# Kernel optimization log

Hardware: AMD Instinct MI355X
Metric: run time of the kernel (lower is better)

## Reference

```python
import jax, jax.numpy as jnp
import numpy as np

d_model = 512


def setup_inputs() -> dict:
    key = jax.random.key(0)
    k1, k2, k3, k4 = jax.random.split(key, 4)
    B, T, d_k = 8, 2048, 64
    scale = 1.0 / np.sqrt(d_model)
    x = jax.random.normal(k1, (B, T, d_model), dtype=jnp.float32)
    Wk = jax.random.normal(k2, (d_model, d_k), dtype=jnp.float32) * scale
    Wq = jax.random.normal(k3, (d_model, d_k), dtype=jnp.float32) * scale
    Wv = jax.random.normal(k4, (d_model, d_k), dtype=jnp.float32) * scale
    return {"x": x, "Wk": Wk, "Wq": Wq, "Wv": Wv}


def reference(x, Wk, Wq, Wv):
    # x: [B,T,C]; W*: [C,d_k]  (torch Linear weight is [d_k,C]; we store transposed)
    k = jnp.einsum('btc,cd->btd', x, Wk)
    q = jnp.einsum('btc,cd->btd', x, Wq)
    v = jnp.einsum('btc,cd->btd', x, Wv)
    d_k = k.shape[-1]
    scores = jnp.einsum('bqd,bkd->bqk', q, k) / jnp.sqrt(jnp.float32(d_k))
    attn = jax.nn.softmax(scores, axis=-1)  # [B,T,T]
    return jnp.einsum('bqk,bkd->bqd', attn, v)
```

## Files before the change

### kernel.cpp

```cpp
#include <hip/hip_runtime.h>
#include <hip/hip_bf16.h>
#include <stdint.h>


typedef short bf16x8 __attribute__((ext_vector_type(8)));
typedef float f32x4 __attribute__((ext_vector_type(4)));

#define MFMA_BF16 __builtin_amdgcn_mfma_f32_16x16x32_bf16

__device__ __forceinline__ unsigned int pk2(float a, float b) {
    __hip_bfloat162 h = __float22bfloat162_rn(float2{a, b});
    union { __hip_bfloat162 h; unsigned int u; } r; r.h = h;
    return r.u;
}

__device__ __forceinline__ uint2 pack4_bf16(float a, float b, float c, float d) {
    uint2 r; r.x = pk2(a, b); r.y = pk2(c, d); return r;
}

__device__ __forceinline__ bf16x8 cvt8(f32x4 a, f32x4 b) {
    union { bf16x8 v; unsigned int u[4]; } r;
    r.u[0] = pk2(a[0], a[1]); r.u[1] = pk2(a[2], a[3]);
    r.u[2] = pk2(b[0], b[1]); r.u[3] = pk2(b[2], b[3]);
    return r.v;
}

__device__ __forceinline__ unsigned short bf1(float a) {
    __hip_bfloat16 h = __float2bfloat16(a);
    union { __hip_bfloat16 h; unsigned short u; } r; r.h = h;
    return r.u;
}

__global__ void wt_kernel(const float* __restrict__ Wq,
                          const float* __restrict__ Wk,
                          const float* __restrict__ Wv,
                          unsigned short* __restrict__ wt2)
{
    int id = blockIdx.x * 256 + threadIdx.x;
    int c    = id & 15;
    int quad = (id >> 4) & 3;
    int ks   = (id >> 6) & 15;
    int mt   = (id >> 10) & 3;
    int w    = id >> 12;
    const float* src = (w == 0) ? Wq : ((w == 1) ? Wk : Wv);
    const int n  = mt * 16 + c;
    const int k0 = ks * 32 + quad * 8;
    unsigned short* dst = wt2 + (size_t)id * 8;
    #pragma unroll
    for (int j = 0; j < 8; j++)
        dst[j] = bf1(src[(size_t)(k0 + j) * 64 + n]);
}

__global__ __launch_bounds__(256, 1) void proj_kernel(
    const float* __restrict__ x, const unsigned short* __restrict__ wt2,
    unsigned short* __restrict__ qg, unsigned short* __restrict__ kg2,
    unsigned short* __restrict__ vg2)
{
    __shared__ unsigned short xs[32768];

    const int tid  = threadIdx.x;
    const int lane = tid & 63;
    const int wave = tid >> 6;
    const int c    = lane & 15;
    const int quad = lane >> 4;
    const int tt   = blockIdx.x;
    const int t0   = tt * 64;

    const float* xb = x + (size_t)tt * 32768;
    #pragma unroll
    for (int t = 0; t < 16; t++) {
        int i = t * 256 + tid;
        f32x4 a = *(const f32x4*)(xb + (size_t)i * 8);
        f32x4 b = *(const f32x4*)(xb + (size_t)i * 8 + 4);
        int tok = i >> 6;
        int db  = i & 63;
        *(bf16x8*)(xs + ((size_t)db * 64 + (tok ^ (db & 7))) * 8) = cvt8(a, b);
    }
    __syncthreads();

    f32x4 acc[3][4];
    #pragma unroll
    for (int r = 0; r < 3; r++)
        #pragma unroll
        for (int st = 0; st < 4; st++) acc[r][st] = f32x4{0.f, 0.f, 0.f, 0.f};

    const int fbase = wave * 3;
    #pragma unroll 2
    for (int ks = 0; ks < 16; ks++) {
        bf16x8 wa[3];
        #pragma unroll
        for (int r = 0; r < 3; r++)
            wa[r] = *(const bf16x8*)(
                wt2 + ((size_t)((fbase + r) * 16 + ks) * 64 + lane) * 8);
        const int sw = c ^ ((ks & 1) * 4 + quad);
        const unsigned short* xrow = xs + ((size_t)(ks * 4 + quad) * 64 + sw) * 8;
        #pragma unroll
        for (int st = 0; st < 4; st++) {
            bf16x8 xf = *(const bf16x8*)(xrow + (size_t)st * 16 * 8);
            #pragma unroll
            for (int r = 0; r < 3; r++)
                acc[r][st] = MFMA_BF16(wa[r], xf, acc[r][st], 0, 0, 0);
        }
    }

    const int b = t0 >> 11;

    #pragma unroll
    for (int r = 0; r < 3; r++) {
        const int f  = fbase + r;
        const int w  = f >> 2;
        const int mt = f & 3;
        #pragma unroll
        for (int st = 0; st < 4; st++) {
            const int ts = t0 + st * 16;
            const int tb = ts & 2047;
            if (w == 0) {
                unsigned short* base = qg + (size_t)(ts + c) * 64;
                *(uint2*)(base + mt * 16 + quad * 4) =
                    pack4_bf16(acc[r][st][0], acc[r][st][1], acc[r][st][2], acc[r][st][3]);
            } else if (w == 1) {
                const int g  = tb >> 4;
                const int h  = mt >> 1;
                const int qk = (mt & 1) * 2 + (quad >> 1);
                size_t chunk = (size_t)b * 16384 + ((size_t)(g * 2 + h) * 4 + qk) * 16 + c;
                *(uint2*)(kg2 + chunk * 8 + (quad & 1) * 4) =
                    pack4_bf16(acc[r][st][0], acc[r][st][1], acc[r][st][2], acc[r][st][3]);
            } else {
                const int tk = tb + c;
                const int s  = tk >> 5;
                const int qv = (tk >> 3) & 3;
                const int j  = tk & 7;
                size_t chunk = (size_t)b * 16384 + ((size_t)(s * 4 + mt) * 4 + qv) * 16 + quad * 4;
                unsigned short* dst = vg2 + chunk * 8 + j;
                dst[0]  = bf1(acc[r][st][0]);
                dst[8]  = bf1(acc[r][st][1]);
                dst[16] = bf1(acc[r][st][2]);
                dst[24] = bf1(acc[r][st][3]);
            }
        }
    }
}

__global__ __launch_bounds__(512, 2) void attn_kernel(
    const unsigned short* __restrict__ qg, const unsigned short* __restrict__ kg2,
    const unsigned short* __restrict__ vg2, float* __restrict__ out)
{
    __shared__ __align__(16) unsigned short pt[8][4][16 * 136];
    __shared__ float lbuf[8][4][16];
    float* obase = reinterpret_cast<float*>(&pt[0][0][0]);

    const int lane = threadIdx.x & 63;
    const int wave = threadIdx.x >> 6;
    const int c    = lane & 15;
    const int quad = lane >> 4;
    const int b    = blockIdx.x & 7;
    const int g    = blockIdx.x >> 3;
    const int tb   = b * 2048 + g * 64;

    unsigned short* ptw = &pt[wave][0][0];
    const unsigned short* kbase = kg2 + ((size_t)b * 16384 + lane) * 8;
    const unsigned short* vbase = vg2 + ((size_t)b * 16384 + lane) * 8;

    bf16x8 qA0 = *(const bf16x8*)(qg + (size_t)(tb + c) * 64 + quad * 8);
    bf16x8 qA1 = *(const bf16x8*)(qg + (size_t)(tb + c) * 64 + 32 + quad * 8);
    bf16x8 qB0 = *(const bf16x8*)(qg + (size_t)(tb + 16 + c) * 64 + quad * 8);
    bf16x8 qB1 = *(const bf16x8*)(qg + (size_t)(tb + 16 + c) * 64 + 32 + quad * 8);
    bf16x8 qC0 = *(const bf16x8*)(qg + (size_t)(tb + 32 + c) * 64 + quad * 8);
    bf16x8 qC1 = *(const bf16x8*)(qg + (size_t)(tb + 32 + c) * 64 + 32 + quad * 8);
    bf16x8 qD0 = *(const bf16x8*)(qg + (size_t)(tb + 48 + c) * 64 + quad * 8);
    bf16x8 qD1 = *(const bf16x8*)(qg + (size_t)(tb + 48 + c) * 64 + 32 + quad * 8);

    f32x4 oa0 = {0,0,0,0}, oa1 = {0,0,0,0}, oa2 = {0,0,0,0}, oa3 = {0,0,0,0};
    f32x4 ob0 = {0,0,0,0}, ob1 = {0,0,0,0}, ob2 = {0,0,0,0}, ob3 = {0,0,0,0};
    f32x4 oc0 = {0,0,0,0}, oc1 = {0,0,0,0}, oc2 = {0,0,0,0}, oc3 = {0,0,0,0};
    f32x4 od0 = {0,0,0,0}, od1 = {0,0,0,0}, od2 = {0,0,0,0}, od3 = {0,0,0,0};
    f32x4 laccA = {0,0,0,0}, laccB = {0,0,0,0};
    f32x4 laccC = {0,0,0,0}, laccD = {0,0,0,0};
    const float cexp = 0.18033688011112042f;

    for (int kt = wave * 2; kt < wave * 2 + 2; kt++) {
        const int key0 = kt * 128;
        const int g0   = key0 >> 4;
        const int s0   = key0 >> 5;
        const f32x4 z = {0,0,0,0};

        f32x4 stA[8], stB[8];
        #pragma unroll
        for (int mt = 0; mt < 8; mt++) {
            bf16x8 k0 = *(const bf16x8*)(kbase + (size_t)((g0 + mt) * 2    ) * 64 * 8);
            bf16x8 k1 = *(const bf16x8*)(kbase + (size_t)((g0 + mt) * 2 + 1) * 64 * 8);
            stA[mt] = MFMA_BF16(k0, qA0, z, 0, 0, 0);
            stA[mt] = MFMA_BF16(k1, qA1, stA[mt], 0, 0, 0);
            stB[mt] = MFMA_BF16(k0, qB0, z, 0, 0, 0);
            stB[mt] = MFMA_BF16(k1, qB1, stB[mt], 0, 0, 0);
        }

        asm volatile("" ::: "memory");
        #pragma unroll
        for (int mt = 0; mt < 8; mt++) {
            float p0 = __builtin_amdgcn_exp2f(stA[mt][0] * cexp);
            float p1 = __builtin_amdgcn_exp2f(stA[mt][1] * cexp);
            float p2 = __builtin_amdgcn_exp2f(stA[mt][2] * cexp);
            float p3 = __builtin_amdgcn_exp2f(stA[mt][3] * cexp);
            laccA[0] += p0; laccA[1] += p1; laccA[2] += p2; laccA[3] += p3;
            *(uint2*)(ptw + c * 136 + mt * 16 + quad * 4) = pack4_bf16(p0, p1, p2, p3);
        }
        #pragma unroll
        for (int mt = 0; mt < 8; mt++) {
            float p0 = __builtin_amdgcn_exp2f(stB[mt][0] * cexp);
            float p1 = __builtin_amdgcn_exp2f(stB[mt][1] * cexp);
            float p2 = __builtin_amdgcn_exp2f(stB[mt][2] * cexp);
            float p3 = __builtin_amdgcn_exp2f(stB[mt][3] * cexp);
            laccB[0] += p0; laccB[1] += p1; laccB[2] += p2; laccB[3] += p3;
            *(uint2*)(ptw + 2176 + c * 136 + mt * 16 + quad * 4) = pack4_bf16(p0, p1, p2, p3);
        }
        asm volatile("" ::: "memory");

        f32x4 stC[8], stD[8];
        #pragma unroll
        for (int mt = 0; mt < 8; mt++) {
            bf16x8 k0 = *(const bf16x8*)(kbase + (size_t)((g0 + mt) * 2    ) * 64 * 8);
            bf16x8 k1 = *(const bf16x8*)(kbase + (size_t)((g0 + mt) * 2 + 1) * 64 * 8);
            stC[mt] = MFMA_BF16(k0, qC0, z, 0, 0, 0);
            stC[mt] = MFMA_BF16(k1, qC1, stC[mt], 0, 0, 0);
            stD[mt] = MFMA_BF16(k0, qD0, z, 0, 0, 0);
            stD[mt] = MFMA_BF16(k1, qD1, stD[mt], 0, 0, 0);
        }

        bf16x8 va[2][4];
        #pragma unroll
        for (int mt = 0; mt < 4; mt++) {
            va[0][mt] = *(const bf16x8*)(vbase + (size_t)((s0    ) * 4 + mt) * 64 * 8);
            va[1][mt] = *(const bf16x8*)(vbase + (size_t)((s0 + 1) * 4 + mt) * 64 * 8);
        }

        asm volatile("" ::: "memory");
        #pragma unroll
        for (int mt = 0; mt < 8; mt++) {
            float p0 = __builtin_amdgcn_exp2f(stC[mt][0] * cexp);
            float p1 = __builtin_amdgcn_exp2f(stC[mt][1] * cexp);
            float p2 = __builtin_amdgcn_exp2f(stC[mt][2] * cexp);
            float p3 = __builtin_amdgcn_exp2f(stC[mt][3] * cexp);
            laccC[0] += p0; laccC[1] += p1; laccC[2] += p2; laccC[3] += p3;
            *(uint2*)(ptw + 2 * 2176 + c * 136 + mt * 16 + quad * 4) = pack4_bf16(p0, p1, p2, p3);
        }
        #pragma unroll
        for (int mt = 0; mt < 8; mt++) {
            float p0 = __builtin_amdgcn_exp2f(stD[mt][0] * cexp);
            float p1 = __builtin_amdgcn_exp2f(stD[mt][1] * cexp);
            float p2 = __builtin_amdgcn_exp2f(stD[mt][2] * cexp);
            float p3 = __builtin_amdgcn_exp2f(stD[mt][3] * cexp);
            laccD[0] += p0; laccD[1] += p1; laccD[2] += p2; laccD[3] += p3;
            *(uint2*)(ptw + 3 * 2176 + c * 136 + mt * 16 + quad * 4) = pack4_bf16(p0, p1, p2, p3);
        }
        asm volatile("" ::: "memory");

        #pragma unroll
        for (int ks = 0; ks < 4; ks++) {
            bf16x8 pbA = *(const bf16x8*)(ptw            + c * 136 + ks * 32 + quad * 8);
            bf16x8 pbB = *(const bf16x8*)(ptw +     2176 + c * 136 + ks * 32 + quad * 8);
            bf16x8 pbC = *(const bf16x8*)(ptw + 2 * 2176 + c * 136 + ks * 32 + quad * 8);
            bf16x8 pbD = *(const bf16x8*)(ptw + 3 * 2176 + c * 136 + ks * 32 + quad * 8);
            bf16x8 v0 = va[ks & 1][0], v1 = va[ks & 1][1];
            bf16x8 v2 = va[ks & 1][2], v3 = va[ks & 1][3];
            if (ks < 2) {
                #pragma unroll
                for (int mt = 0; mt < 4; mt++)
                    va[ks & 1][mt] =
                        *(const bf16x8*)(vbase + (size_t)((s0 + ks + 2) * 4 + mt) * 64 * 8);
            }
            oa0 = MFMA_BF16(v0, pbA, oa0, 0, 0, 0);
            oa1 = MFMA_BF16(v1, pbA, oa1, 0, 0, 0);
            oa2 = MFMA_BF16(v2, pbA, oa2, 0, 0, 0);
            oa3 = MFMA_BF16(v3, pbA, oa3, 0, 0, 0);
            ob0 = MFMA_BF16(v0, pbB, ob0, 0, 0, 0);
            ob1 = MFMA_BF16(v1, pbB, ob1, 0, 0, 0);
            ob2 = MFMA_BF16(v2, pbB, ob2, 0, 0, 0);
            ob3 = MFMA_BF16(v3, pbB, ob3, 0, 0, 0);
            oc0 = MFMA_BF16(v0, pbC, oc0, 0, 0, 0);
            oc1 = MFMA_BF16(v1, pbC, oc1, 0, 0, 0);
            oc2 = MFMA_BF16(v2, pbC, oc2, 0, 0, 0);
            oc3 = MFMA_BF16(v3, pbC, oc3, 0, 0, 0);
            od0 = MFMA_BF16(v0, pbD, od0, 0, 0, 0);
            od1 = MFMA_BF16(v1, pbD, od1, 0, 0, 0);
            od2 = MFMA_BF16(v2, pbD, od2, 0, 0, 0);
            od3 = MFMA_BF16(v3, pbD, od3, 0, 0, 0);
        }
        asm volatile("" ::: "memory");
    }

    float lA = (laccA[0] + laccA[1]) + (laccA[2] + laccA[3]);
    lA += __shfl_xor(lA, 16); lA += __shfl_xor(lA, 32);
    float lB = (laccB[0] + laccB[1]) + (laccB[2] + laccB[3]);
    lB += __shfl_xor(lB, 16); lB += __shfl_xor(lB, 32);
    float lC = (laccC[0] + laccC[1]) + (laccC[2] + laccC[3]);
    lC += __shfl_xor(lC, 16); lC += __shfl_xor(lC, 32);
    float lD = (laccD[0] + laccD[1]) + (laccD[2] + laccD[3]);
    lD += __shfl_xor(lD, 16); lD += __shfl_xor(lD, 32);
    if (quad == 0) {
        lbuf[wave][0][c] = lA; lbuf[wave][1][c] = lB;
        lbuf[wave][2][c] = lC; lbuf[wave][3][c] = lD;
    }

    __syncthreads();

    if (wave < 4) {
        float* o0 = obase + ((size_t)(wave * 4 + 0) * 16 + c) * 68 + quad * 4;
        float* o1 = obase + ((size_t)(wave * 4 + 1) * 16 + c) * 68 + quad * 4;
        float* o2 = obase + ((size_t)(wave * 4 + 2) * 16 + c) * 68 + quad * 4;
        float* o3 = obase + ((size_t)(wave * 4 + 3) * 16 + c) * 68 + quad * 4;
        *(f32x4*)(o0 +  0) = oa0; *(f32x4*)(o0 + 16) = oa1;
        *(f32x4*)(o0 + 32) = oa2; *(f32x4*)(o0 + 48) = oa3;
        *(f32x4*)(o1 +  0) = ob0; *(f32x4*)(o1 + 16) = ob1;
        *(f32x4*)(o1 + 32) = ob2; *(f32x4*)(o1 + 48) = ob3;
        *(f32x4*)(o2 +  0) = oc0; *(f32x4*)(o2 + 16) = oc1;
        *(f32x4*)(o2 + 32) = oc2; *(f32x4*)(o2 + 48) = oc3;
        *(f32x4*)(o3 +  0) = od0; *(f32x4*)(o3 + 16) = od1;
        *(f32x4*)(o3 + 32) = od2; *(f32x4*)(o3 + 48) = od3;
    }
    __syncthreads();

    if (wave >= 4) {
        const int p = wave - 4;
        float* o0 = obase + ((size_t)(p * 4 + 0) * 16 + c) * 68 + quad * 4;
        float* o1 = obase + ((size_t)(p * 4 + 1) * 16 + c) * 68 + quad * 4;
        float* o2 = obase + ((size_t)(p * 4 + 2) * 16 + c) * 68 + quad * 4;
        float* o3 = obase + ((size_t)(p * 4 + 3) * 16 + c) * 68 + quad * 4;
        #define ADDSTORE(ptr, off, reg) { f32x4 t = *(f32x4*)((ptr) + (off)); \
            t[0] += reg[0]; t[1] += reg[1]; t[2] += reg[2]; t[3] += reg[3];   \
            *(f32x4*)((ptr) + (off)) = t; }
        ADDSTORE(o0,  0, oa0); ADDSTORE(o0, 16, oa1);
        ADDSTORE(o0, 32, oa2); ADDSTORE(o0, 48, oa3);
        ADDSTORE(o1,  0, ob0); ADDSTORE(o1, 16, ob1);
        ADDSTORE(o1, 32, ob2); ADDSTORE(o1, 48, ob3);
        ADDSTORE(o2,  0, oc0); ADDSTORE(o2, 16, oc1);
        ADDSTORE(o2, 32, oc2); ADDSTORE(o2, 48, oc3);
        ADDSTORE(o3,  0, od0); ADDSTORE(o3, 16, od1);
        ADDSTORE(o3, 32, od2); ADDSTORE(o3, 48, od3);
        #undef ADDSTORE
    }
    __syncthreads();

    const int tid = threadIdx.x;
    const int row = tid >> 3;
    const int d0  = (tid & 7) * 8;
    const int qt  = row >> 4;
    const int r   = row & 15;
    float L = 0.f;
    #pragma unroll
    for (int w = 0; w < 8; w++) L += lbuf[w][qt][r];
    const float rl = 1.f / L;
    f32x4 Oa = {0,0,0,0}, Ob = {0,0,0,0};
    #pragma unroll
    for (int p = 0; p < 4; p++) {
        const float* src = obase + ((size_t)(p * 4 + qt) * 16 + r) * 68 + d0;
        f32x4 a   = *(const f32x4*)(src);
        f32x4 bfr = *(const f32x4*)(src + 4);
        Oa[0] += a[0]; Oa[1] += a[1]; Oa[2] += a[2]; Oa[3] += a[3];
        Ob[0] += bfr[0]; Ob[1] += bfr[1]; Ob[2] += bfr[2]; Ob[3] += bfr[3];
    }
    Oa[0] *= rl; Oa[1] *= rl; Oa[2] *= rl; Oa[3] *= rl;
    Ob[0] *= rl; Ob[1] *= rl; Ob[2] *= rl; Ob[3] *= rl;
    float* op = out + (size_t)(tb + row) * 64 + d0;
    *(f32x4*)op       = Oa;
    *(f32x4*)(op + 4) = Ob;
}

extern "C" void kernel_launch(void* const* d_in, const int* in_sizes, int n_in,
                              void* d_out, int out_size, void* d_ws, size_t ws_size,
                              hipStream_t stream)
{
    const float* x  = (const float*)d_in[0];
    const float* Wk = (const float*)d_in[1];
    const float* Wq = (const float*)d_in[2];
    const float* Wv = (const float*)d_in[3];
    float* out = (float*)d_out;

    char* ws = (char*)d_ws;
    unsigned short* qg  = (unsigned short*)(ws);
    unsigned short* kg2 = (unsigned short*)(ws + (2u << 20));
    unsigned short* vg2 = (unsigned short*)(ws + (4u << 20));
    unsigned short* wt2 = (unsigned short*)(ws + (6u << 20));

    hipLaunchKernelGGL(wt_kernel,   dim3(48),   dim3(256), 0, stream,
                       Wq, Wk, Wv, wt2);
    hipLaunchKernelGGL(proj_kernel, dim3(256),  dim3(256), 0, stream,
                       x, wt2, qg, kg2, vg2);
    hipLaunchKernelGGL(attn_kernel, dim3(256),  dim3(512), 0, stream,
                       qg, kg2, vg2, out);
}
```

Before: 106.3 us.

## Fold softmax scale into Q, compute row sums via MFMA, merge score loops

```diff
diff --git a/kernel.cpp b/kernel.cpp
--- a/kernel.cpp
+++ b/kernel.cpp
@@ -7,6 +7,8 @@
 typedef float f32x4 __attribute__((ext_vector_type(4)));
 
 #define MFMA_BF16 __builtin_amdgcn_mfma_f32_16x16x32_bf16
+
+#define CEXP 0.18033688011112042f
 
 __device__ __forceinline__ unsigned int pk2(float a, float b) {
     __hip_bfloat162 h = __float22bfloat162_rn(float2{a, b});
@@ -117,7 +119,8 @@
             if (w == 0) {
                 unsigned short* base = qg + (size_t)(ts + c) * 64;
                 *(uint2*)(base + mt * 16 + quad * 4) =
-                    pack4_bf16(acc[r][st][0], acc[r][st][1], acc[r][st][2], acc[r][st][3]);
+                    pack4_bf16(acc[r][st][0] * CEXP, acc[r][st][1] * CEXP,
+                               acc[r][st][2] * CEXP, acc[r][st][3] * CEXP);
             } else if (w == 1) {
                 const int g  = tb >> 4;
                 const int h  = mt >> 1;
@@ -170,13 +173,16 @@
     bf16x8 qD0 = *(const bf16x8*)(qg + (size_t)(tb + 48 + c) * 64 + quad * 8);
     bf16x8 qD1 = *(const bf16x8*)(qg + (size_t)(tb + 48 + c) * 64 + 32 + quad * 8);
 
+    bf16x8 ones;
+    #pragma unroll
+    for (int j = 0; j < 8; j++) ones[j] = (short)0x3F80;
+
     f32x4 oa0 = {0,0,0,0}, oa1 = {0,0,0,0}, oa2 = {0,0,0,0}, oa3 = {0,0,0,0};
     f32x4 ob0 = {0,0,0,0}, ob1 = {0,0,0,0}, ob2 = {0,0,0,0}, ob3 = {0,0,0,0};
     f32x4 oc0 = {0,0,0,0}, oc1 = {0,0,0,0}, oc2 = {0,0,0,0}, oc3 = {0,0,0,0};
     f32x4 od0 = {0,0,0,0}, od1 = {0,0,0,0}, od2 = {0,0,0,0}, od3 = {0,0,0,0};
     f32x4 laccA = {0,0,0,0}, laccB = {0,0,0,0};
     f32x4 laccC = {0,0,0,0}, laccD = {0,0,0,0};
-    const float cexp = 0.18033688011112042f;
 
     for (int kt = wave * 2; kt < wave * 2 + 2; kt++) {
         const int key0 = kt * 128;
@@ -184,74 +190,37 @@
         const int s0   = key0 >> 5;
         const f32x4 z = {0,0,0,0};
 
-        f32x4 stA[8], stB[8];
+        bf16x8 va[2][4];
+        #pragma unroll
+        for (int mt = 0; mt < 4; mt++) {
+            va[0][mt] = *(const bf16x8*)(vbase + (size_t)((s0    ) * 4 + mt) * 64 * 8);
+            va[1][mt] = *(const bf16x8*)(vbase + (size_t)((s0 + 1) * 4 + mt) * 64 * 8);
+        }
+
         #pragma unroll
         for (int mt = 0; mt < 8; mt++) {
             bf16x8 k0 = *(const bf16x8*)(kbase + (size_t)((g0 + mt) * 2    ) * 64 * 8);
             bf16x8 k1 = *(const bf16x8*)(kbase + (size_t)((g0 + mt) * 2 + 1) * 64 * 8);
-            stA[mt] = MFMA_BF16(k0, qA0, z, 0, 0, 0);
-            stA[mt] = MFMA_BF16(k1, qA1, stA[mt], 0, 0, 0);
-            stB[mt] = MFMA_BF16(k0, qB0, z, 0, 0, 0);
-            stB[mt] = MFMA_BF16(k1, qB1, stB[mt], 0, 0, 0);
-        }
-
-        asm volatile("" ::: "memory");
-        #pragma unroll
-        for (int mt = 0; mt < 8; mt++) {
-            float p0 = __builtin_amdgcn_exp2f(stA[mt][0] * cexp);
-            float p1 = __builtin_amdgcn_exp2f(stA[mt][1] * cexp);
-            float p2 = __builtin_amdgcn_exp2f(stA[mt][2] * cexp);
-            float p3 = __builtin_amdgcn_exp2f(stA[mt][3] * cexp);
-            laccA[0] += p0; laccA[1] += p1; laccA[2] += p2; laccA[3] += p3;
-            *(uint2*)(ptw + c * 136 + mt * 16 + quad * 4) = pack4_bf16(p0, p1, p2, p3);
-        }
-        #pragma unroll
-        for (int mt = 0; mt < 8; mt++) {
-            float p0 = __builtin_amdgcn_exp2f(stB[mt][0] * cexp);
-            float p1 = __builtin_amdgcn_exp2f(stB[mt][1] * cexp);
-            float p2 = __builtin_amdgcn_exp2f(stB[mt][2] * cexp);
-            float p3 = __builtin_amdgcn_exp2f(stB[mt][3] * cexp);
-            laccB[0] += p0; laccB[1] += p1; laccB[2] += p2; laccB[3] += p3;
-            *(uint2*)(ptw + 2176 + c * 136 + mt * 16 + quad * 4) = pack4_bf16(p0, p1, p2, p3);
-        }
-        asm volatile("" ::: "memory");
-
-        f32x4 stC[8], stD[8];
-        #pragma unroll
-        for (int mt = 0; mt < 8; mt++) {
-            bf16x8 k0 = *(const bf16x8*)(kbase + (size_t)((g0 + mt) * 2    ) * 64 * 8);
-            bf16x8 k1 = *(const bf16x8*)(kbase + (size_t)((g0 + mt) * 2 + 1) * 64 * 8);
-            stC[mt] = MFMA_BF16(k0, qC0, z, 0, 0, 0);
-            stC[mt] = MFMA_BF16(k1, qC1, stC[mt], 0, 0, 0);
-            stD[mt] = MFMA_BF16(k0, qD0, z, 0, 0, 0);
-            stD[mt] = MFMA_BF16(k1, qD1, stD[mt], 0, 0, 0);
-        }
-
-        bf16x8 va[2][4];
-        #pragma unroll
-        for (int mt = 0; mt < 4; mt++) {
-            va[0][mt] = *(const bf16x8*)(vbase + (size_t)((s0    ) * 4 + mt) * 64 * 8);
-            va[1][mt] = *(const bf16x8*)(vbase + (size_t)((s0 + 1) * 4 + mt) * 64 * 8);
-        }
-
-        asm volatile("" ::: "memory");
-        #pragma unroll
-        for (int mt = 0; mt < 8; mt++) {
-            float p0 = __builtin_amdgcn_exp2f(stC[mt][0] * cexp);
-            float p1 = __builtin_amdgcn_exp2f(stC[mt][1] * cexp);
-            float p2 = __builtin_amdgcn_exp2f(stC[mt][2] * cexp);
-            float p3 = __builtin_amdgcn_exp2f(stC[mt][3] * cexp);
-            laccC[0] += p0; laccC[1] += p1; laccC[2] += p2; laccC[3] += p3;
-            *(uint2*)(ptw + 2 * 2176 + c * 136 + mt * 16 + quad * 4) = pack4_bf16(p0, p1, p2, p3);
-        }
-        #pragma unroll
-        for (int mt = 0; mt < 8; mt++) {
-            float p0 = __builtin_amdgcn_exp2f(stD[mt][0] * cexp);
-            float p1 = __builtin_amdgcn_exp2f(stD[mt][1] * cexp);
-            float p2 = __builtin_amdgcn_exp2f(stD[mt][2] * cexp);
-            float p3 = __builtin_amdgcn_exp2f(stD[mt][3] * cexp);
-            laccD[0] += p0; laccD[1] += p1; laccD[2] += p2; laccD[3] += p3;
-            *(uint2*)(ptw + 3 * 2176 + c * 136 + mt * 16 + quad * 4) = pack4_bf16(p0, p1, p2, p3);
+            f32x4 sA = MFMA_BF16(k0, qA0, z, 0, 0, 0);
+            sA = MFMA_BF16(k1, qA1, sA, 0, 0, 0);
+            f32x4 sB = MFMA_BF16(k0, qB0, z, 0, 0, 0);
+            sB = MFMA_BF16(k1, qB1, sB, 0, 0, 0);
+            f32x4 sC = MFMA_BF16(k0, qC0, z, 0, 0, 0);
+            sC = MFMA_BF16(k1, qC1, sC, 0, 0, 0);
+            f32x4 sD = MFMA_BF16(k0, qD0, z, 0, 0, 0);
+            sD = MFMA_BF16(k1, qD1, sD, 0, 0, 0);
+            *(uint2*)(ptw            + c * 136 + mt * 16 + quad * 4) =
+                pack4_bf16(__builtin_amdgcn_exp2f(sA[0]), __builtin_amdgcn_exp2f(sA[1]),
+                           __builtin_amdgcn_exp2f(sA[2]), __builtin_amdgcn_exp2f(sA[3]));
+            *(uint2*)(ptw +     2176 + c * 136 + mt * 16 + quad * 4) =
+                pack4_bf16(__builtin_amdgcn_exp2f(sB[0]), __builtin_amdgcn_exp2f(sB[1]),
+                           __builtin_amdgcn_exp2f(sB[2]), __builtin_amdgcn_exp2f(sB[3]));
+            *(uint2*)(ptw + 2 * 2176 + c * 136 + mt * 16 + quad * 4) =
+                pack4_bf16(__builtin_amdgcn_exp2f(sC[0]), __builtin_amdgcn_exp2f(sC[1]),
+                           __builtin_amdgcn_exp2f(sC[2]), __builtin_amdgcn_exp2f(sC[3]));
+            *(uint2*)(ptw + 3 * 2176 + c * 136 + mt * 16 + quad * 4) =
+                pack4_bf16(__builtin_amdgcn_exp2f(sD[0]), __builtin_amdgcn_exp2f(sD[1]),
+                           __builtin_amdgcn_exp2f(sD[2]), __builtin_amdgcn_exp2f(sD[3]));
         }
         asm volatile("" ::: "memory");
 
@@ -273,33 +242,29 @@
             oa1 = MFMA_BF16(v1, pbA, oa1, 0, 0, 0);
             oa2 = MFMA_BF16(v2, pbA, oa2, 0, 0, 0);
             oa3 = MFMA_BF16(v3, pbA, oa3, 0, 0, 0);
+            laccA = MFMA_BF16(ones, pbA, laccA, 0, 0, 0);
             ob0 = MFMA_BF16(v0, pbB, ob0, 0, 0, 0);
             ob1 = MFMA_BF16(v1, pbB, ob1, 0, 0, 0);
             ob2 = MFMA_BF16(v2, pbB, ob2, 0, 0, 0);
             ob3 = MFMA_BF16(v3, pbB, ob3, 0, 0, 0);
+            laccB = MFMA_BF16(ones, pbB, laccB, 0, 0, 0);
             oc0 = MFMA_BF16(v0, pbC, oc0, 0, 0, 0);
             oc1 = MFMA_BF16(v1, pbC, oc1, 0, 0, 0);
             oc2 = MFMA_BF16(v2, pbC, oc2, 0, 0, 0);
             oc3 = MFMA_BF16(v3, pbC, oc3, 0, 0, 0);
+            laccC = MFMA_BF16(ones, pbC, laccC, 0, 0, 0);
             od0 = MFMA_BF16(v0, pbD, od0, 0, 0, 0);
             od1 = MFMA_BF16(v1, pbD, od1, 0, 0, 0);
             od2 = MFMA_BF16(v2, pbD, od2, 0, 0, 0);
             od3 = MFMA_BF16(v3, pbD, od3, 0, 0, 0);
+            laccD = MFMA_BF16(ones, pbD, laccD, 0, 0, 0);
         }
         asm volatile("" ::: "memory");
     }
 
-    float lA = (laccA[0] + laccA[1]) + (laccA[2] + laccA[3]);
-    lA += __shfl_xor(lA, 16); lA += __shfl_xor(lA, 32);
-    float lB = (laccB[0] + laccB[1]) + (laccB[2] + laccB[3]);
-    lB += __shfl_xor(lB, 16); lB += __shfl_xor(lB, 32);
-    float lC = (laccC[0] + laccC[1]) + (laccC[2] + laccC[3]);
-    lC += __shfl_xor(lC, 16); lC += __shfl_xor(lC, 32);
-    float lD = (laccD[0] + laccD[1]) + (laccD[2] + laccD[3]);
-    lD += __shfl_xor(lD, 16); lD += __shfl_xor(lD, 32);
     if (quad == 0) {
-        lbuf[wave][0][c] = lA; lbuf[wave][1][c] = lB;
-        lbuf[wave][2][c] = lC; lbuf[wave][3][c] = lD;
+        lbuf[wave][0][c] = laccA[0]; lbuf[wave][1][c] = laccB[0];
+        lbuf[wave][2][c] = laccC[0]; lbuf[wave][3][c] = laccD[0];
     }
 
     __syncthreads();
```

Result: faster. 102.3 us (median of 2 runs) (-3.8%).
